# Kernel optimization log

Hardware: AMD Instinct MI355X
Metric: run time of the kernel (lower is better)

The kernel has to match this reference:

```python
import jax, jax.numpy as jnp
import numpy as np

DIM = 1024
HEADS = 16
DIM_HEAD = 64
B = 4
N = 2048
INNER = HEADS * DIM_HEAD
SCALE = DIM_HEAD ** -0.5
NEG = -1e9


def setup_inputs() -> dict:
    key = jax.random.key(0)
    k1, k2, k3 = jax.random.split(key, 3)
    x = jax.random.normal(k1, (B, N, DIM), dtype=jnp.float32)
    w_qkv = jax.random.normal(k2, (DIM, 3 * INNER), dtype=jnp.float32) * (DIM ** -0.5)
    w_out = jax.random.normal(k3, (INNER, DIM), dtype=jnp.float32) * (INNER ** -0.5)
    b_out = jnp.zeros((DIM,), dtype=jnp.float32)
    return {"x": x, "w_qkv": w_qkv, "w_out": w_out, "b_out": b_out}


def reference(x, w_qkv, w_out, b_out):
    b, n, _ = x.shape
    qkv = x @ w_qkv  # [b, n, 3*inner]
    q, k, v = jnp.split(qkv, 3, axis=-1)
    # [b, n, inner] -> [b, h, n, d]
    split_heads = lambda t: t.reshape(b, n, HEADS, DIM_HEAD).transpose(0, 2, 1, 3)
    q, k, v = split_heads(q), split_heads(k), split_heads(v)
    dots = jnp.einsum('bhid,bhjd->bhij', q, k) * SCALE
    causal = jnp.tril(jnp.ones((n, n), dtype=bool))  # mask[i,j]=1 for j<=i
    dots = jnp.where(causal, dots, NEG)
    attn = jax.nn.softmax(dots, axis=-1)
    out = jnp.einsum('bhij,bhjd->bhid', attn, v)
    out = out.transpose(0, 2, 1, 3).reshape(b, n, INNER)
    return out @ w_out + b_out
```

## Files before the change

kernel.cpp:

```cpp
#include <hip/hip_runtime.h>

typedef unsigned short u16;
typedef unsigned int u32;
typedef __attribute__((ext_vector_type(8))) short short8;
typedef __attribute__((ext_vector_type(4))) float f32x4;
typedef __attribute__((ext_vector_type(4))) short short4v;
typedef __attribute__((ext_vector_type(2))) unsigned int uint2v;

#define MFMA_BF16(a, b, c) __builtin_amdgcn_mfma_f32_16x16x32_bf16((a), (b), (c), 0, 0, 0)

__device__ __forceinline__ void gl2lds16(const u16* g, u16* l) {
  __builtin_amdgcn_global_load_lds(
      (const __attribute__((address_space(1))) unsigned int*)g,
      (__attribute__((address_space(3))) unsigned int*)l, 16, 0, 0);
}

__device__ __forceinline__ u16 f2bf(float f) {
  union { float f; unsigned u; } v; v.f = f;
  unsigned r = v.u + 0x7fffu + ((v.u >> 16) & 1u);
  return (u16)(r >> 16);
}

__device__ __forceinline__ u32 pack_bf16(float a, float b) {
  __bf16 ha = (__bf16)a, hb = (__bf16)b;
  u16 ua, ub;
  __builtin_memcpy(&ua, &ha, 2);
  __builtin_memcpy(&ub, &hb, 2);
  return (u32)ua | ((u32)ub << 16);
}

__device__ __forceinline__ void cfence() { asm volatile("" ::: "memory"); }

__device__ __forceinline__ float fast_exp2(float x) {
#if __has_builtin(__builtin_amdgcn_exp2f)
  return __builtin_amdgcn_exp2f(x);
#else
  return __expf(x * 0.6931471805599453f);
#endif
}

__device__ __forceinline__ u32 swz(u32 x) { return x ^ (((x >> 7) & 7u) << 4); }

__global__ void fill_one_f32(float* p, int n) {
  int i = blockIdx.x * blockDim.x + threadIdx.x;
  if (i < n) p[i] = 1.0f;
}

__global__ void prep_k(const float* __restrict__ x, u16* __restrict__ Xb,
                       const float* __restrict__ w_qkv, u16* __restrict__ wqkvT,
                       const float* __restrict__ w_out, u16* __restrict__ woutT) {
  __shared__ float tile[32][33];
  const int bid = blockIdx.x, t = threadIdx.x;
  if (bid < 2048) {
    const int base = (bid * 256 + t) * 16;
#pragma unroll
    for (int h = 0; h < 2; ++h) {
      const f32x4 v0 = *(const f32x4*)&x[base + h * 8];
      const f32x4 v1 = *(const f32x4*)&x[base + h * 8 + 4];
      short8 o;
      o[0] = (short)f2bf(v0.x); o[1] = (short)f2bf(v0.y);
      o[2] = (short)f2bf(v0.z); o[3] = (short)f2bf(v0.w);
      o[4] = (short)f2bf(v1.x); o[5] = (short)f2bf(v1.y);
      o[6] = (short)f2bf(v1.z); o[7] = (short)f2bf(v1.w);
      *(short8*)&Xb[base + h * 8] = o;
    }
    return;
  }
  const float* src; u16* dst; int R, C, bx, by;
  if (bid < 5120) {
    const int tb = bid - 2048;
    src = w_qkv; dst = wqkvT; R = 1024; C = 3072; bx = tb % 96; by = tb / 96;
  } else {
    const int tb = bid - 5120;
    src = w_out; dst = woutT; R = 1024; C = 1024; bx = tb % 32; by = tb / 32;
  }
  const int tx = t & 31, ty = t >> 5;
  const int r0 = by * 32, c0 = bx * 32;
#pragma unroll
  for (int i = 0; i < 4; ++i)
    tile[ty + i * 8][tx] = src[(size_t)(r0 + ty + i * 8) * C + c0 + tx];
  __syncthreads();
#pragma unroll
  for (int i = 0; i < 4; ++i)
    dst[(size_t)(c0 + ty + i * 8) * R + r0 + tx] = f2bf(tile[tx][ty + i * 8]);
}

template <int MODE>
__launch_bounds__(256, 2)
__global__ void gemm_bt_k(const u16* __restrict__ A, const u16* __restrict__ Bt,
                          int K, int Ncols,
                          u16* __restrict__ O0, u16* __restrict__ O1,
                          u16* __restrict__ O2,
                          float* __restrict__ Of, const float* __restrict__ biasf) {
  __shared__ __align__(16) u16 Al[3 * 4096];
  __shared__ __align__(16) u16 Bl[3 * 4096];
  const int t = threadIdx.x;
  const int w = t >> 6, l = t & 63;
  const int quad = l >> 4, l16 = l & 15;
  const int m0 = blockIdx.y * 128, n0 = blockIdx.x * 128;
  const int wm = w & 1, wn = w >> 1;

  f32x4 acc[4][4];
#pragma unroll
  for (int a = 0; a < 4; ++a)
#pragma unroll
    for (int b = 0; b < 4; ++b) acc[a][b] = (f32x4){0.f, 0.f, 0.f, 0.f};

  const u32 o0 = (u32)t * 16u, o1 = o0 + 4096u;
  const u32 l0 = swz(o0), l1 = swz(o1 & 8191u);
  const u32 rA0 = (l0 >> 7) * 2 + ((l0 >> 6) & 1), q0 = (l0 >> 4) & 3u;
  const u32 rA1 = (l1 >> 7) * 2 + ((l1 >> 6) & 1), q1 = (l1 >> 4) & 3u;
  const u16* srcA0 = A + (size_t)(m0 + rA0) * K + q0 * 8;
  const u16* srcA1 = A + (size_t)(m0 + rA1) * K + q1 * 8;
  const u16* srcB0 = Bt + (size_t)(n0 + rA0) * K + q0 * 8;
  const u16* srcB1 = Bt + (size_t)(n0 + rA1) * K + q1 * 8;

#define STAGE(kel_, s_)                                      \
  do {                                                       \
    char* _da = (char*)(Al + (s_)*4096);                     \
    char* _db = (char*)(Bl + (s_)*4096);                     \
    gl2lds16(srcA0 + (kel_), (u16*)(_da + o0));              \
    gl2lds16(srcA1 + (kel_), (u16*)(_da + o1));              \
    gl2lds16(srcB0 + (kel_), (u16*)(_db + o0));              \
    gl2lds16(srcB1 + (kel_), (u16*)(_db + o1));              \
  } while (0)

  u32 sa[4], sb[4];
#pragma unroll
  for (int a = 0; a < 4; ++a) {
    const u32 row = wm * 64 + a * 16 + l16;
    sa[a] = swz(((row >> 1) << 7) | ((row & 1) << 6) | ((u32)quad << 4));
  }
#pragma unroll
  for (int b = 0; b < 4; ++b) {
    const u32 row = wn * 64 + b * 16 + l16;
    sb[b] = swz(((row >> 1) << 7) | ((row & 1) << 6) | ((u32)quad << 4));
  }

  const int NT = K >> 5;

  STAGE(0, 0);
  STAGE(32, 1);
  asm volatile("s_waitcnt vmcnt(4)" ::: "memory");
  cfence(); __builtin_amdgcn_s_barrier(); cfence();

  int rd = 0, st = 2;
  int kel = 64;
#pragma unroll 1
  for (int tt = 0; tt < NT - 2; ++tt) {
    STAGE(kel, st);
    kel += 32;
    const char* ca = (const char*)(Al + rd * 4096);
    const char* cb = (const char*)(Bl + rd * 4096);
    short8 av[4], bv[4];
#pragma unroll
    for (int a = 0; a < 4; ++a) av[a] = *(const short8*)(ca + sa[a]);
#pragma unroll
    for (int b = 0; b < 4; ++b) bv[b] = *(const short8*)(cb + sb[b]);
    __builtin_amdgcn_s_setprio(1);
#pragma unroll
    for (int a = 0; a < 4; ++a)
#pragma unroll
      for (int b = 0; b < 4; ++b)
        acc[a][b] = MFMA_BF16(av[a], bv[b], acc[a][b]);
    __builtin_amdgcn_s_setprio(0);
    asm volatile("s_waitcnt vmcnt(4)" ::: "memory");
    cfence(); __builtin_amdgcn_s_barrier(); cfence();
    rd = (rd == 2) ? 0 : rd + 1;
    st = (st == 2) ? 0 : st + 1;
  }
  {
    const char* ca = (const char*)(Al + rd * 4096);
    const char* cb = (const char*)(Bl + rd * 4096);
    short8 av[4], bv[4];
#pragma unroll
    for (int a = 0; a < 4; ++a) av[a] = *(const short8*)(ca + sa[a]);
#pragma unroll
    for (int b = 0; b < 4; ++b) bv[b] = *(const short8*)(cb + sb[b]);
#pragma unroll
    for (int a = 0; a < 4; ++a)
#pragma unroll
      for (int b = 0; b < 4; ++b)
        acc[a][b] = MFMA_BF16(av[a], bv[b], acc[a][b]);
    asm volatile("s_waitcnt vmcnt(0)" ::: "memory");
    cfence(); __builtin_amdgcn_s_barrier(); cfence();
    rd = (rd == 2) ? 0 : rd + 1;
  }
  {
    const char* ca = (const char*)(Al + rd * 4096);
    const char* cb = (const char*)(Bl + rd * 4096);
    short8 av[4], bv[4];
#pragma unroll
    for (int a = 0; a < 4; ++a) av[a] = *(const short8*)(ca + sa[a]);
#pragma unroll
    for (int b = 0; b < 4; ++b) bv[b] = *(const short8*)(cb + sb[b]);
#pragma unroll
    for (int a = 0; a < 4; ++a)
#pragma unroll
      for (int b = 0; b < 4; ++b)
        acc[a][b] = MFMA_BF16(av[a], bv[b], acc[a][b]);
  }
#undef STAGE

#pragma unroll
  for (int a = 0; a < 4; ++a)
#pragma unroll
    for (int b = 0; b < 4; ++b) {
      const int row0 = m0 + wm * 64 + a * 16 + quad * 4;
      const int col = n0 + wn * 64 + b * 16 + l16;
      if (MODE == 0) {
        const int bb = row0 >> 11, n = row0 & 2047;
        const int which = col >> 10, j = col & 1023, h = j >> 6, d = j & 63;
        if (which == 2) {
          short4v o;
#pragma unroll
          for (int r = 0; r < 4; ++r) o[r] = (short)f2bf(acc[a][b][r]);
          *(short4v*)&O2[(((size_t)bb * 16 + h) * 64 + d) * 2048 + n] = o;
        } else {
          u16* dst = which ? O1 : O0;
#pragma unroll
          for (int r = 0; r < 4; ++r)
            dst[(((size_t)bb * 16 + h) * 2048 + (n + r)) * 64 + d] =
                f2bf(acc[a][b][r]);
        }
      } else {
#pragma unroll
        for (int r = 0; r < 4; ++r)
          Of[(size_t)(row0 + r) * Ncols + col] = acc[a][b][r] + biasf[col];
      }
    }
}

__launch_bounds__(512, 2)
__global__ void flash_k11(const u16* __restrict__ Q, const u16* __restrict__ K,
                          const u16* __restrict__ VT, u16* __restrict__ AO) {
  __shared__ __align__(16) u16 Klds[2][64 * 64];
  __shared__ __align__(16) u16 Vt[2][64 * 64];
  __shared__ __align__(16) u16 Plds[8][16 * 64];
  const int t = threadIdx.x, w = t >> 6, l = t & 63;
  const int quad = l >> 4, l16 = l & 15;
  const int flat = blockIdx.x;
  const int bh = flat & 63;
  const int grp = flat >> 6;
  const int qi = (grp < 4) ? grp : (11 - grp);
  const size_t base = (size_t)bh * 2048 * 64;
  const u16* Qp = Q + base;
  const u16* Kp = K + base;
  const u16* VTp = VT + base;
  const int bb = bh >> 4, hh = bh & 15;
  const float SC2 = 0.18033688011112042f;
  const float FM2 = -4.328085122666891f;

  const int kcp = t >> 3;
  const int kcd = (t & 7) * 8;
  const u32 stoff = swz((u32)(kcp * 128 + (t & 7) * 16));

  short8 ones;
#pragma unroll
  for (int j = 0; j < 8; ++j) ones[j] = (short)0x3F80;

  const int qbase = qi * 256;

  short8 qf[2][2];
#pragma unroll
  for (int mi = 0; mi < 2; ++mi) {
    const int qrow = qbase + w * 32 + mi * 16 + l16;
    qf[mi][0] = *(const short8*)&Qp[(size_t)qrow * 64 + quad * 8];
    qf[mi][1] = *(const short8*)&Qp[(size_t)qrow * 64 + 32 + quad * 8];
  }

  u32 koff0[4], koff1[4];
#pragma unroll
  for (int nf = 0; nf < 4; ++nf) {
    const u32 pre = (u32)((nf * 16 + l16) * 128 + quad * 16);
    koff0[nf] = swz(pre);
    koff1[nf] = koff0[nf] ^ 64u;
  }
  u32 pwoff[4];
#pragma unroll
  for (int nf = 0; nf < 4; ++nf)
    pwoff[nf] = swz((u32)(l16 * 128 + nf * 32 + quad * 8));
  const u32 proff0 = swz((u32)(l16 * 128 + quad * 16));
  const u32 proff1 = proff0 ^ 64u;

  f32x4 oacc[2][4], lacc[2];
#pragma unroll
  for (int mi = 0; mi < 2; ++mi) {
    lacc[mi] = (f32x4){0.f, 0.f, 0.f, 0.f};
#pragma unroll
    for (int df = 0; df < 4; ++df) oacc[mi][df] = (f32x4){0.f, 0.f, 0.f, 0.f};
  }

  const int nkt = 4 * qi + 4;
  const int wlo = qbase + w * 32;
  const int whi = wlo + 31;

  short8 kv = *(const short8*)&Kp[(size_t)kcp * 64 + kcd];
  short8 vv = *(const short8*)&VTp[(size_t)kcp * 2048 + kcd];

#pragma unroll 1
  for (int kt = 0; kt < nkt; ++kt) {
    const int buf = kt & 1;
    *(short8*)((char*)Klds[buf] + stoff) = kv;
    *(short8*)((char*)Vt[buf] + stoff) = vv;
    __syncthreads();

    if (kt + 1 < nkt) {
      kv = *(const short8*)&Kp[(size_t)((kt + 1) * 64 + kcp) * 64 + kcd];
      vv = *(const short8*)&VTp[(size_t)kcp * 2048 + (kt + 1) * 64 + kcd];
    }

    const bool skip = (kt * 64 > whi);
    if (!skip) {
      f32x4 sa[2][4];
#pragma unroll
      for (int nf = 0; nf < 4; ++nf) {
        const char* kb = (const char*)Klds[buf];
        const short8 kf0 = *(const short8*)(kb + koff0[nf]);
        const short8 kf1 = *(const short8*)(kb + koff1[nf]);
#pragma unroll
        for (int mi = 0; mi < 2; ++mi) {
          f32x4 s = (f32x4){0.f, 0.f, 0.f, 0.f};
          s = MFMA_BF16(kf0, qf[mi][0], s);
          s = MFMA_BF16(kf1, qf[mi][1], s);
          sa[mi][nf] = s;
        }
      }

      const bool needmask = (kt * 64 + 63 > wlo);
      short8 pf[2][2];
#pragma unroll
      for (int mi = 0; mi < 2; ++mi) {
        const int qrow = qbase + w * 32 + mi * 16 + l16;
        char* pw = (char*)Plds[w];
#pragma unroll
        for (int nf = 0; nf < 4; ++nf) {
          float pe[4];
#pragma unroll
          for (int r = 0; r < 4; ++r) {
            float arg = fmaf(sa[mi][nf][r], SC2, FM2);
            if (needmask) {
              const int kp = kt * 64 + nf * 16 + quad * 4 + r;
              arg = (kp <= qrow) ? arg : -1e9f;
            }
            pe[r] = fast_exp2(arg);
          }
          *(uint2v*)(pw + pwoff[nf]) =
              (uint2v){pack_bf16(pe[0], pe[1]), pack_bf16(pe[2], pe[3])};
        }
        pf[mi][0] = *(const short8*)(pw + proff0);
        pf[mi][1] = *(const short8*)(pw + proff1);
        lacc[mi] = MFMA_BF16(pf[mi][0], ones, lacc[mi]);
        lacc[mi] = MFMA_BF16(pf[mi][1], ones, lacc[mi]);
      }

#pragma unroll
      for (int df = 0; df < 4; ++df) {
        const char* vb = (const char*)Vt[buf];
        const short8 vf0 = *(const short8*)(vb + koff0[df]);
        const short8 vf1 = *(const short8*)(vb + koff1[df]);
#pragma unroll
        for (int mi = 0; mi < 2; ++mi) {
          oacc[mi][df] = MFMA_BF16(pf[mi][0], vf0, oacc[mi][df]);
          oacc[mi][df] = MFMA_BF16(pf[mi][1], vf1, oacc[mi][df]);
        }
      }
    }
  }

#pragma unroll
  for (int mi = 0; mi < 2; ++mi) {
    const int srow = qbase + w * 32 + mi * 16 + quad * 4;
#pragma unroll
    for (int df = 0; df < 4; ++df)
#pragma unroll
      for (int r = 0; r < 4; ++r) {
        const int n = srow + r;
        const int d = df * 16 + l16;
        AO[((size_t)bb * 2048 + n) * 1024 + hh * 64 + d] =
            f2bf(oacc[mi][df][r] / lacc[mi][r]);
      }
  }
}

extern "C" void kernel_launch(void* const* d_in, const int* in_sizes, int n_in,
                              void* d_out, int out_size, void* d_ws, size_t ws_size,
                              hipStream_t stream) {
  const float* x = (const float*)d_in[0];
  const float* w_qkv = (const float*)d_in[1];
  const float* w_out = (const float*)d_in[2];
  const float* b_out = (const float*)d_in[3];
  float* out = (float*)d_out;

  const size_t MB = 1024 * 1024;
  if (ws_size < 72 * MB) {
    fill_one_f32<<<(out_size + 255) / 256, 256, 0, stream>>>(out, out_size);
    return;
  }

  char* ws = (char*)d_ws;
  u16* wqkvT = (u16*)(ws);
  u16* woutT = (u16*)(ws + 6 * MB);
  u16* Xb = (u16*)(ws + 8 * MB);
  u16* AO = Xb;
  u16* Qb = (u16*)(ws + 24 * MB);
  u16* Kb = (u16*)(ws + 40 * MB);
  u16* VbT = (u16*)(ws + 56 * MB);

  prep_k<<<6144, 256, 0, stream>>>(x, Xb, w_qkv, wqkvT, w_out, woutT);
  gemm_bt_k<0><<<dim3(3072 / 128, 8192 / 128), 256, 0, stream>>>(
      Xb, wqkvT, 1024, 3072, Qb, Kb, VbT, nullptr, nullptr);
  flash_k11<<<512, 512, 0, stream>>>(Qb, Kb, VbT, AO);
  gemm_bt_k<1><<<dim3(1024 / 128, 8192 / 128), 256, 0, stream>>>(
      AO, woutT, 1024, 1024, nullptr, nullptr, nullptr, out, b_out);
}
```

Before: 253.1 us.

## Pair complementary causal query tiles per flash block to share K/V loads

Each flash-attention block now processes two query tiles, p and 7-p, so every block does the same amount of causal work. The K/V tiles staged in LDS are reused by both query tiles. The grid halves from 512 to 256 blocks, and s_setprio is raised around the MFMA sections. This removes redundant K/V loads for the short tile and the load imbalance from the causal triangle. In exchange it doubles accumulator and Q-fragment register pressure, uses more LDS for P, and leaves only 256 blocks on a GPU with many CUs, which may hurt occupancy.

```diff
diff --git a/kernel.cpp b/kernel.cpp
--- a/kernel.cpp
+++ b/kernel.cpp
@@ -232,17 +232,16 @@
 }
 
 __launch_bounds__(512, 2)
-__global__ void flash_k11(const u16* __restrict__ Q, const u16* __restrict__ K,
+__global__ void flash_k12(const u16* __restrict__ Q, const u16* __restrict__ K,
                           const u16* __restrict__ VT, u16* __restrict__ AO) {
   __shared__ __align__(16) u16 Klds[2][64 * 64];
   __shared__ __align__(16) u16 Vt[2][64 * 64];
-  __shared__ __align__(16) u16 Plds[8][16 * 64];
+  __shared__ __align__(16) u16 Plds[8][2][16 * 64];
   const int t = threadIdx.x, w = t >> 6, l = t & 63;
   const int quad = l >> 4, l16 = l & 15;
   const int flat = blockIdx.x;
   const int bh = flat & 63;
-  const int grp = flat >> 6;
-  const int qi = (grp < 4) ? grp : (11 - grp);
+  const int p = flat >> 6;
   const size_t base = (size_t)bh * 2048 * 64;
   const u16* Qp = Q + base;
   const u16* Kp = K + base;
@@ -251,6 +250,8 @@
   const float SC2 = 0.18033688011112042f;
   const float FM2 = -4.328085122666891f;
 
+  const int qbase[2] = {p * 256, (7 - p) * 256};
+
   const int kcp = t >> 3;
   const int kcd = (t & 7) * 8;
   const u32 stoff = swz((u32)(kcp * 128 + (t & 7) * 16));
@@ -259,15 +260,15 @@
 #pragma unroll
   for (int j = 0; j < 8; ++j) ones[j] = (short)0x3F80;
 
-  const int qbase = qi * 256;
-
-  short8 qf[2][2];
-#pragma unroll
-  for (int mi = 0; mi < 2; ++mi) {
-    const int qrow = qbase + w * 32 + mi * 16 + l16;
-    qf[mi][0] = *(const short8*)&Qp[(size_t)qrow * 64 + quad * 8];
-    qf[mi][1] = *(const short8*)&Qp[(size_t)qrow * 64 + 32 + quad * 8];
-  }
+  short8 qf[2][2][2];
+#pragma unroll
+  for (int ql = 0; ql < 2; ++ql)
+#pragma unroll
+    for (int mi = 0; mi < 2; ++mi) {
+      const int qrow = qbase[ql] + w * 32 + mi * 16 + l16;
+      qf[ql][mi][0] = *(const short8*)&Qp[(size_t)qrow * 64 + quad * 8];
+      qf[ql][mi][1] = *(const short8*)&Qp[(size_t)qrow * 64 + 32 + quad * 8];
+    }
 
   u32 koff0[4], koff1[4];
 #pragma unroll
@@ -283,104 +284,116 @@
   const u32 proff0 = swz((u32)(l16 * 128 + quad * 16));
   const u32 proff1 = proff0 ^ 64u;
 
-  f32x4 oacc[2][4], lacc[2];
-#pragma unroll
-  for (int mi = 0; mi < 2; ++mi) {
-    lacc[mi] = (f32x4){0.f, 0.f, 0.f, 0.f};
-#pragma unroll
-    for (int df = 0; df < 4; ++df) oacc[mi][df] = (f32x4){0.f, 0.f, 0.f, 0.f};
-  }
-
-  const int nkt = 4 * qi + 4;
-  const int wlo = qbase + w * 32;
-  const int whi = wlo + 31;
+  f32x4 oacc[2][2][4], lacc[2][2];
+#pragma unroll
+  for (int ql = 0; ql < 2; ++ql)
+#pragma unroll
+    for (int mi = 0; mi < 2; ++mi) {
+      lacc[ql][mi] = (f32x4){0.f, 0.f, 0.f, 0.f};
+#pragma unroll
+      for (int df = 0; df < 4; ++df)
+        oacc[ql][mi][df] = (f32x4){0.f, 0.f, 0.f, 0.f};
+    }
+
+  const int nktMax = 4 * (7 - p) + 4;
+  const int wlo[2] = {qbase[0] + w * 32, qbase[1] + w * 32};
+  const int whi[2] = {wlo[0] + 31, wlo[1] + 31};
 
   short8 kv = *(const short8*)&Kp[(size_t)kcp * 64 + kcd];
   short8 vv = *(const short8*)&VTp[(size_t)kcp * 2048 + kcd];
 
 #pragma unroll 1
-  for (int kt = 0; kt < nkt; ++kt) {
+  for (int kt = 0; kt < nktMax; ++kt) {
     const int buf = kt & 1;
     *(short8*)((char*)Klds[buf] + stoff) = kv;
     *(short8*)((char*)Vt[buf] + stoff) = vv;
     __syncthreads();
 
-    if (kt + 1 < nkt) {
+    if (kt + 1 < nktMax) {
       kv = *(const short8*)&Kp[(size_t)((kt + 1) * 64 + kcp) * 64 + kcd];
       vv = *(const short8*)&VTp[(size_t)kcp * 2048 + (kt + 1) * 64 + kcd];
     }
 
-    const bool skip = (kt * 64 > whi);
-    if (!skip) {
-      f32x4 sa[2][4];
-#pragma unroll
-      for (int nf = 0; nf < 4; ++nf) {
-        const char* kb = (const char*)Klds[buf];
-        const short8 kf0 = *(const short8*)(kb + koff0[nf]);
-        const short8 kf1 = *(const short8*)(kb + koff1[nf]);
+#pragma unroll
+    for (int ql = 0; ql < 2; ++ql) {
+      const bool skip = (kt * 64 > whi[ql]);
+      if (!skip) {
+        f32x4 sa[2][4];
+        __builtin_amdgcn_s_setprio(1);
+#pragma unroll
+        for (int nf = 0; nf < 4; ++nf) {
+          const char* kb = (const char*)Klds[buf];
+          const short8 kf0 = *(const short8*)(kb + koff0[nf]);
+          const short8 kf1 = *(const short8*)(kb + koff1[nf]);
+#pragma unroll
+          for (int mi = 0; mi < 2; ++mi) {
+            f32x4 s = (f32x4){0.f, 0.f, 0.f, 0.f};
+            s = MFMA_BF16(kf0, qf[ql][mi][0], s);
+            s = MFMA_BF16(kf1, qf[ql][mi][1], s);
+            sa[mi][nf] = s;
+          }
+        }
+        __builtin_amdgcn_s_setprio(0);
+
+        const bool needmask = (kt * 64 + 63 > wlo[ql]);
+        short8 pf[2][2];
 #pragma unroll
         for (int mi = 0; mi < 2; ++mi) {
-          f32x4 s = (f32x4){0.f, 0.f, 0.f, 0.f};
-          s = MFMA_BF16(kf0, qf[mi][0], s);
-          s = MFMA_BF16(kf1, qf[mi][1], s);
-          sa[mi][nf] = s;
+          const int qrow = qbase[ql] + w * 32 + mi * 16 + l16;
+          char* pw = (char*)Plds[w][ql];
+#pragma unroll
+          for (int nf = 0; nf < 4; ++nf) {
+            float pe[4];
+#pragma unroll
+            for (int r = 0; r < 4; ++r) {
+              float arg = fmaf(sa[mi][nf][r], SC2, FM2);
+              if (needmask) {
+                const int kp = kt * 64 + nf * 16 + quad * 4 + r;
+                arg = (kp <= qrow) ? arg : -1e9f;
+              }
+              pe[r] = fast_exp2(arg);
+            }
+            *(uint2v*)(pw + pwoff[nf]) =
+                (uint2v){pack_bf16(pe[0], pe[1]), pack_bf16(pe[2], pe[3])};
+          }
+          pf[mi][0] = *(const short8*)(pw + proff0);
+          pf[mi][1] = *(const short8*)(pw + proff1);
+          lacc[ql][mi] = MFMA_BF16(pf[mi][0], ones, lacc[ql][mi]);
+          lacc[ql][mi] = MFMA_BF16(pf[mi][1], ones, lacc[ql][mi]);
         }
+
+        __builtin_amdgcn_s_setprio(1);
+#pragma unroll
+        for (int df = 0; df < 4; ++df) {
+          const char* vb = (const char*)Vt[buf];
+          const short8 vf0 = *(const short8*)(vb + koff0[df]);
+          const short8 vf1 = *(const short8*)(vb + koff1[df]);
+#pragma unroll
+          for (int mi = 0; mi < 2; ++mi) {
+            oacc[ql][mi][df] = MFMA_BF16(pf[mi][0], vf0, oacc[ql][mi][df]);
+            oacc[ql][mi][df] = MFMA_BF16(pf[mi][1], vf1, oacc[ql][mi][df]);
+          }
+        }
+        __builtin_amdgcn_s_setprio(0);
       }
-
-      const bool needmask = (kt * 64 + 63 > wlo);
-      short8 pf[2][2];
-#pragma unroll
-      for (int mi = 0; mi < 2; ++mi) {
-        const int qrow = qbase + w * 32 + mi * 16 + l16;
-        char* pw = (char*)Plds[w];
-#pragma unroll
-        for (int nf = 0; nf < 4; ++nf) {
-          float pe[4];
-#pragma unroll
-          for (int r = 0; r < 4; ++r) {
-            float arg = fmaf(sa[mi][nf][r], SC2, FM2);
-            if (needmask) {
-              const int kp = kt * 64 + nf * 16 + quad * 4 + r;
-              arg = (kp <= qrow) ? arg : -1e9f;
-            }
-            pe[r] = fast_exp2(arg);
-          }
-          *(uint2v*)(pw + pwoff[nf]) =
-              (uint2v){pack_bf16(pe[0], pe[1]), pack_bf16(pe[2], pe[3])};
+    }
+  }
+
+#pragma unroll
+  for (int ql = 0; ql < 2; ++ql)
+#pragma unroll
+    for (int mi = 0; mi < 2; ++mi) {
+      const int srow = qbase[ql] + w * 32 + mi * 16 + quad * 4;
+#pragma unroll
+      for (int df = 0; df < 4; ++df)
+#pragma unroll
+        for (int r = 0; r < 4; ++r) {
+          const int n = srow + r;
+          const int d = df * 16 + l16;
+          AO[((size_t)bb * 2048 + n) * 1024 + hh * 64 + d] =
+              f2bf(oacc[ql][mi][df][r] / lacc[ql][mi][r]);
         }
-        pf[mi][0] = *(const short8*)(pw + proff0);
-        pf[mi][1] = *(const short8*)(pw + proff1);
-        lacc[mi] = MFMA_BF16(pf[mi][0], ones, lacc[mi]);
-        lacc[mi] = MFMA_BF16(pf[mi][1], ones, lacc[mi]);
-      }
-
-#pragma unroll
-      for (int df = 0; df < 4; ++df) {
-        const char* vb = (const char*)Vt[buf];
-        const short8 vf0 = *(const short8*)(vb + koff0[df]);
-        const short8 vf1 = *(const short8*)(vb + koff1[df]);
-#pragma unroll
-        for (int mi = 0; mi < 2; ++mi) {
-          oacc[mi][df] = MFMA_BF16(pf[mi][0], vf0, oacc[mi][df]);
-          oacc[mi][df] = MFMA_BF16(pf[mi][1], vf1, oacc[mi][df]);
-        }
-      }
-    }
-  }
-
-#pragma unroll
-  for (int mi = 0; mi < 2; ++mi) {
-    const int srow = qbase + w * 32 + mi * 16 + quad * 4;
-#pragma unroll
-    for (int df = 0; df < 4; ++df)
-#pragma unroll
-      for (int r = 0; r < 4; ++r) {
-        const int n = srow + r;
-        const int d = df * 16 + l16;
-        AO[((size_t)bb * 2048 + n) * 1024 + hh * 64 + d] =
-            f2bf(oacc[mi][df][r] / lacc[mi][r]);
-      }
-  }
+    }
 }
 
 extern "C" void kernel_launch(void* const* d_in, const int* in_sizes, int n_in,
@@ -410,7 +423,7 @@
   prep_k<<<6144, 256, 0, stream>>>(x, Xb, w_qkv, wqkvT, w_out, woutT);
   gemm_bt_k<0><<<dim3(3072 / 128, 8192 / 128), 256, 0, stream>>>(
       Xb, wqkvT, 1024, 3072, Qb, Kb, VbT, nullptr, nullptr);
-  flash_k11<<<512, 512, 0, stream>>>(Qb, Kb, VbT, AO);
+  flash_k12<<<256, 512, 0, stream>>>(Qb, Kb, VbT, AO);
   gemm_bt_k<1><<<dim3(1024 / 128, 8192 / 128), 256, 0, stream>>>(
       AO, woutT, 1024, 1024, nullptr, nullptr, nullptr, out, b_out);
 }
```

Result: no change. 253.9 us (+0.3%).

## Split flash attention blocks into 128-row halves and raise MFMA priority

Applied to the files above, without the earlier changes.

The attention kernel now uses 256-thread blocks that each handle 128 query rows instead of 512-thread blocks covering 256 rows, launching 1024 blocks. Each block stops its key loop at its own half's causal limit and drops the reversed query-block ordering. Each thread now stages two K and V chunks per tile. s_setprio is raised around the MFMA sections so matrix work gets issue priority over the softmax phase. Smaller blocks give finer load balance across the causal triangle and more resident blocks, but each K/V tile is loaded by twice as many blocks, which adds global traffic.

```diff
diff --git a/kernel.cpp b/kernel.cpp
--- a/kernel.cpp
+++ b/kernel.cpp
@@ -231,18 +231,19 @@
     }
 }
 
-__launch_bounds__(512, 2)
-__global__ void flash_k11(const u16* __restrict__ Q, const u16* __restrict__ K,
+__launch_bounds__(256, 3)
+__global__ void flash_k13(const u16* __restrict__ Q, const u16* __restrict__ K,
                           const u16* __restrict__ VT, u16* __restrict__ AO) {
   __shared__ __align__(16) u16 Klds[2][64 * 64];
   __shared__ __align__(16) u16 Vt[2][64 * 64];
-  __shared__ __align__(16) u16 Plds[8][16 * 64];
+  __shared__ __align__(16) u16 Plds[4][16 * 64];
   const int t = threadIdx.x, w = t >> 6, l = t & 63;
   const int quad = l >> 4, l16 = l & 15;
   const int flat = blockIdx.x;
   const int bh = flat & 63;
-  const int grp = flat >> 6;
-  const int qi = (grp < 4) ? grp : (11 - grp);
+  const int qih = flat >> 6;
+  const int qi = qih >> 1, hf = qih & 1;
+  const int qbase = qi * 256 + hf * 128;
   const size_t base = (size_t)bh * 2048 * 64;
   const u16* Qp = Q + base;
   const u16* Kp = K + base;
@@ -253,13 +254,12 @@
 
   const int kcp = t >> 3;
   const int kcd = (t & 7) * 8;
-  const u32 stoff = swz((u32)(kcp * 128 + (t & 7) * 16));
+  const u32 st0 = swz((u32)(kcp * 128 + (t & 7) * 16));
+  const u32 st1 = swz((u32)((kcp + 32) * 128 + (t & 7) * 16));
 
   short8 ones;
 #pragma unroll
   for (int j = 0; j < 8; ++j) ones[j] = (short)0x3F80;
-
-  const int qbase = qi * 256;
 
   short8 qf[2][2];
 #pragma unroll
@@ -291,28 +291,35 @@
     for (int df = 0; df < 4; ++df) oacc[mi][df] = (f32x4){0.f, 0.f, 0.f, 0.f};
   }
 
-  const int nkt = 4 * qi + 4;
+  const int nkt = 4 * qi + 2 * hf + 2;
   const int wlo = qbase + w * 32;
   const int whi = wlo + 31;
 
-  short8 kv = *(const short8*)&Kp[(size_t)kcp * 64 + kcd];
-  short8 vv = *(const short8*)&VTp[(size_t)kcp * 2048 + kcd];
+  short8 kv0 = *(const short8*)&Kp[(size_t)kcp * 64 + kcd];
+  short8 kv1 = *(const short8*)&Kp[(size_t)(kcp + 32) * 64 + kcd];
+  short8 vv0 = *(const short8*)&VTp[(size_t)kcp * 2048 + kcd];
+  short8 vv1 = *(const short8*)&VTp[(size_t)(kcp + 32) * 2048 + kcd];
 
 #pragma unroll 1
   for (int kt = 0; kt < nkt; ++kt) {
     const int buf = kt & 1;
-    *(short8*)((char*)Klds[buf] + stoff) = kv;
-    *(short8*)((char*)Vt[buf] + stoff) = vv;
+    *(short8*)((char*)Klds[buf] + st0) = kv0;
+    *(short8*)((char*)Klds[buf] + st1) = kv1;
+    *(short8*)((char*)Vt[buf] + st0) = vv0;
+    *(short8*)((char*)Vt[buf] + st1) = vv1;
     __syncthreads();
 
     if (kt + 1 < nkt) {
-      kv = *(const short8*)&Kp[(size_t)((kt + 1) * 64 + kcp) * 64 + kcd];
-      vv = *(const short8*)&VTp[(size_t)kcp * 2048 + (kt + 1) * 64 + kcd];
+      kv0 = *(const short8*)&Kp[(size_t)((kt + 1) * 64 + kcp) * 64 + kcd];
+      kv1 = *(const short8*)&Kp[(size_t)((kt + 1) * 64 + kcp + 32) * 64 + kcd];
+      vv0 = *(const short8*)&VTp[(size_t)kcp * 2048 + (kt + 1) * 64 + kcd];
+      vv1 = *(const short8*)&VTp[(size_t)(kcp + 32) * 2048 + (kt + 1) * 64 + kcd];
     }
 
     const bool skip = (kt * 64 > whi);
     if (!skip) {
       f32x4 sa[2][4];
+      __builtin_amdgcn_s_setprio(1);
 #pragma unroll
       for (int nf = 0; nf < 4; ++nf) {
         const char* kb = (const char*)Klds[buf];
@@ -326,6 +333,7 @@
           sa[mi][nf] = s;
         }
       }
+      __builtin_amdgcn_s_setprio(0);
 
       const bool needmask = (kt * 64 + 63 > wlo);
       short8 pf[2][2];
@@ -354,6 +362,7 @@
         lacc[mi] = MFMA_BF16(pf[mi][1], ones, lacc[mi]);
       }
 
+      __builtin_amdgcn_s_setprio(1);
 #pragma unroll
       for (int df = 0; df < 4; ++df) {
         const char* vb = (const char*)Vt[buf];
@@ -365,6 +374,7 @@
           oacc[mi][df] = MFMA_BF16(pf[mi][1], vf1, oacc[mi][df]);
         }
       }
+      __builtin_amdgcn_s_setprio(0);
     }
   }
 
@@ -410,7 +420,7 @@
   prep_k<<<6144, 256, 0, stream>>>(x, Xb, w_qkv, wqkvT, w_out, woutT);
   gemm_bt_k<0><<<dim3(3072 / 128, 8192 / 128), 256, 0, stream>>>(
       Xb, wqkvT, 1024, 3072, Qb, Kb, VbT, nullptr, nullptr);
-  flash_k11<<<512, 512, 0, stream>>>(Qb, Kb, VbT, AO);
+  flash_k13<<<1024, 256, 0, stream>>>(Qb, Kb, VbT, AO);
   gemm_bt_k<1><<<dim3(1024 / 128, 8192 / 128), 256, 0, stream>>>(
       AO, woutT, 1024, 1024, nullptr, nullptr, nullptr, out, b_out);
 }
```

Result: slower. 260.7 us (+3.0%).
